# Performance work log

Measured on AMD Instinct MI355X. Metric: run time of the kernel, lower is better.

## Reference

```python
import jax, jax.numpy as jnp
import numpy as np

B, T, C = 64, 1024, 32   # batch, seq_len, n_embd
H, D = 4, 8              # num_heads, head_size (H*D == C)


def setup_inputs() -> dict:
    key = jax.random.key(0)
    ks = jax.random.split(key, 6)
    s = 0.02  # init scale for weights
    x = jax.random.normal(ks[0], (B, T, C), dtype=jnp.float32)
    Wq = jax.random.normal(ks[1], (H, C, D), dtype=jnp.float32) * s
    Wk = jax.random.normal(ks[2], (H, C, D), dtype=jnp.float32) * s
    Wv = jax.random.normal(ks[3], (H, C, D), dtype=jnp.float32) * s
    Wproj = jax.random.normal(ks[4], (H * D, C), dtype=jnp.float32) * s
    bproj = jnp.zeros((C,), dtype=jnp.float32)
    return {"x": x, "Wq": Wq, "Wk": Wk, "Wv": Wv, "Wproj": Wproj, "bproj": bproj}


def reference(x, Wq, Wk, Wv, Wproj, bproj):
    # All heads batched into one einsum instead of a Python loop over Head modules.
    q = jnp.einsum('btc,hcd->bhtd', x, Wq)
    k = jnp.einsum('btc,hcd->bhtd', x, Wk)
    v = jnp.einsum('btc,hcd->bhtd', x, Wv)
    scale = D ** -0.5
    att = jnp.einsum('bhtd,bhsd->bhts', q, k) * scale  # [B,H,T,T]
    causal = jnp.tril(jnp.ones((T, T), dtype=bool))
    att = jnp.where(causal, att, jnp.float32(-1e9))
    att = jax.nn.softmax(att, axis=-1)  # dropout omitted (eval mode)
    o = jnp.einsum('bhts,bhsd->bhtd', att, v)
    o = o.transpose(0, 2, 1, 3).reshape(B, T, H * D)  # concat heads on last dim
    return o @ Wproj + bproj  # final proj; output dropout omitted (eval mode)
```

## Files before the change

### kernel.cpp

```cpp
#include <hip/hip_runtime.h>
#include <math.h>

static constexpr int Bb = 64, Tt = 1024, Cc = 32, Hh = 4, Dd = 8;
static constexpr float QSCALE = 0.51006973f;

typedef _Float16 h2  __attribute__((ext_vector_type(2)));
typedef _Float16 v4h __attribute__((ext_vector_type(4)));
typedef float  f32x4 __attribute__((ext_vector_type(4)));

__device__ __forceinline__ h2 pkrtz(float a, float b) {
  return __builtin_bit_cast(h2, __builtin_amdgcn_cvt_pkrtz(a, b));
}

__device__ __forceinline__ float fdot2(h2 a, h2 b, float c) {
#if __has_builtin(__builtin_amdgcn_fdot2)
  return __builtin_amdgcn_fdot2(a, b, c, false);
#else
  return fmaf((float)a.x, (float)b.x, fmaf((float)a.y, (float)b.y, c));
#endif
}

__device__ __forceinline__ float frcp(float x) {
#if __has_builtin(__builtin_amdgcn_rcpf)
  return __builtin_amdgcn_rcpf(x);
#else
  return 1.0f / x;
#endif
}

__device__ __forceinline__ float bperm_f32(int src_lane, float v) {
  return __builtin_bit_cast(float,
      __builtin_amdgcn_ds_bpermute(src_lane << 2, __builtin_bit_cast(int, v)));
}

__device__ __forceinline__ h2 exp2h2(h2 s) {
  const h2 A3 = {(_Float16)0.05550411f, (_Float16)0.05550411f};
  const h2 A2 = {(_Float16)0.24022651f, (_Float16)0.24022651f};
  const h2 A1 = {(_Float16)0.69314718f, (_Float16)0.69314718f};
  const h2 ONE = {(_Float16)1.0f, (_Float16)1.0f};
  h2 t = A3 * s + A2;
  t = t * s + A1;
  t = t * s + ONE;
  return t;
}

union U4 { uint4 u; h2 h[4]; };
union P2 { uint2 u; h2 h[2]; v4h v; };

__global__ __launch_bounds__(256) void qkv_kernel(
    const float* __restrict__ x, const float* __restrict__ Wq,
    const float* __restrict__ Wk, const float* __restrict__ Wv,
    ushort* __restrict__ qo, ushort* __restrict__ ko, ushort* __restrict__ vo)
{
  __shared__ h2 wT[3][Hh][Dd][16];
  const int tid = threadIdx.x;
  {
    const int sh = tid >> 6, sd = (tid >> 3) & 7, c2b = tid & 7;
    const float* Ws[3] = {Wq, Wk, Wv};
#pragma unroll
    for (int mat = 0; mat < 3; ++mat) {
      const float* W = Ws[mat];
#pragma unroll
      for (int i = 0; i < 2; ++i) {
        const int c2 = c2b + 8 * i;
        const float w0 = W[(sh * Cc + 2 * c2) * Dd + sd];
        const float w1 = W[(sh * Cc + 2 * c2 + 1) * Dd + sd];
        wT[mat][sh][sd][c2] = pkrtz(w0, w1);
      }
    }
  }
  __syncthreads();

  const int h = tid >> 6, lane = tid & 63;
  const int b = blockIdx.x >> 3;
  const int t0 = ((blockIdx.x & 7) << 7) + lane;
  const int t1 = t0 + 64;
  const int bh = b * Hh + h;

  h2 xa[16], xb[16];
  {
    const float4* g0 = (const float4*)(x + ((long)b * Tt + t0) * Cc);
    const float4* g1 = (const float4*)(x + ((long)b * Tt + t1) * Cc);
#pragma unroll
    for (int i = 0; i < 8; ++i) {
      float4 va = g0[i], vb = g1[i];
      xa[2 * i]     = pkrtz(va.x, va.y);
      xa[2 * i + 1] = pkrtz(va.z, va.w);
      xb[2 * i]     = pkrtz(vb.x, vb.y);
      xb[2 * i + 1] = pkrtz(vb.z, vb.w);
    }
  }

#pragma unroll
  for (int mat = 0; mat < 3; ++mat) {
    float a0[Dd], a1[Dd];
#pragma unroll
    for (int d = 0; d < Dd; ++d) {
      float s0 = 0.f, s1 = 0.f;
#pragma unroll
      for (int c2 = 0; c2 < 16; ++c2) {
        const h2 w = wT[mat][h][d][c2];
        s0 = fdot2(xa[c2], w, s0);
        s1 = fdot2(xb[c2], w, s1);
      }
      a0[d] = s0; a1[d] = s1;
    }
    if (mat == 2) {
#pragma unroll
      for (int d = 0; d < Dd; ++d) {
        ((_Float16*)vo)[((long)bh * Dd + d) * Tt + t0] = (_Float16)a0[d];
        ((_Float16*)vo)[((long)bh * Dd + d) * Tt + t1] = (_Float16)a1[d];
      }
    } else {
      const float sc = (mat == 0) ? QSCALE : 1.0f;
      ushort* dst = (mat == 0) ? qo : ko;
      U4 u0, u1;
#pragma unroll
      for (int i = 0; i < 4; ++i) {
        u0.h[i] = pkrtz(a0[2 * i] * sc, a0[2 * i + 1] * sc);
        u1.h[i] = pkrtz(a1[2 * i] * sc, a1[2 * i + 1] * sc);
      }
      ((uint4*)(dst + ((long)bh * Tt + t0) * Dd))[0] = u0.u;
      ((uint4*)(dst + ((long)bh * Tt + t1) * Dd))[0] = u1.u;
    }
  }
}

__global__ __launch_bounds__(256, 4) void flash_kernel(
    const ushort* __restrict__ qg, const ushort* __restrict__ kg,
    const ushort* __restrict__ vg, ushort* __restrict__ og)
{
  __shared__ __align__(16) ushort ks[Tt * Dd];
  __shared__ __align__(16) ushort vs[9 * 1032];
  const int tid = threadIdx.x;
  const int bh = blockIdx.x & 255;
  const int g  = blockIdx.x >> 8;

  {
    const uint4* ksrc = (const uint4*)(kg + (long)bh * Tt * Dd);
    const uint4* vsrc = (const uint4*)(vg + (long)bh * Dd * Tt);
#pragma unroll
    for (int i = 0; i < 4; ++i)
      ((uint4*)ks)[tid + 256 * i] = ksrc[tid + 256 * i];
#pragma unroll
    for (int i = 0; i < 4; ++i) {
      const int idx = tid + 256 * i;
      const int d = idx >> 7, c8 = idx & 127;
      *(uint4*)(vs + d * 1032 + c8 * 8) = vsrc[idx];
    }
    if (tid < 128) {
      const unsigned one2 = 0x3C003C00u;
      *(uint4*)(vs + 8 * 1032 + tid * 8) = make_uint4(one2, one2, one2, one2);
    }
  }
  __syncthreads();

  const int lane = tid & 63;
  const int u  = __builtin_amdgcn_readfirstlane(tid >> 6);
  const int up = g * 4 + u;
  int rb[4];
  rb[0] = up; rb[1] = 31 - up; rb[2] = 32 + up; rb[3] = 63 - up;

  const int n = lane & 15, quad = lane >> 4;
  const ushort* kbase = ks + n * Dd + (quad & 1) * 4;
  const int vr = (n <= 8) ? n : (n - 8);
  const ushort* vbase = vs + vr * 1032 + quad * 4;

  h2 km0 = {(_Float16)((4 * quad + 0) <= n ? 1.f : 0.f),
            (_Float16)((4 * quad + 1) <= n ? 1.f : 0.f)};
  h2 km1 = {(_Float16)((4 * quad + 2) <= n ? 1.f : 0.f),
            (_Float16)((4 * quad + 3) <= n ? 1.f : 0.f)};

  P2 bq[4];
#pragma unroll
  for (int i = 0; i < 4; ++i) {
    uint2 r = *(const uint2*)(qg + ((long)bh * Tt + rb[i] * 16 + n) * Dd + (quad & 1) * 4);
    if (quad & 2) { r.x = 0; r.y = 0; }
    bq[i].u = r;
  }

  const f32x4 zero4 = {0.f, 0.f, 0.f, 0.f};
  f32x4 o[4];
#pragma unroll
  for (int i = 0; i < 4; ++i) o[i] = zero4;

  const int ctmax = 63 - up;
#pragma unroll 1
  for (int ct = 0; ct <= ctmax; ++ct) {
    P2 ak; ak.u = *(const uint2*)(kbase + ct * 128);
    const v4h bv = *(const v4h*)(vbase + ct * 16);
#pragma unroll
    for (int i = 0; i < 4; ++i) {
      if (ct <= rb[i]) {
        f32x4 s = __builtin_amdgcn_mfma_f32_16x16x16f16(ak.v, bq[i].v, zero4, 0, 0, 0);
        h2 p0 = exp2h2(pkrtz(s[0], s[1]));
        h2 p1 = exp2h2(pkrtz(s[2], s[3]));
        if (ct == rb[i]) { p0 *= km0; p1 *= km1; }
        P2 pf; pf.h[0] = p0; pf.h[1] = p1;
        o[i] = __builtin_amdgcn_mfma_f32_16x16x16f16(pf.v, bv, o[i], 0, 0, 0);
      }
    }
  }

  const int b = bh >> 2, h = bh & 3;
  const int lsrc = (lane & 48) | 8;
#pragma unroll
  for (int i = 0; i < 4; ++i) {
#pragma unroll
    for (int r = 0; r < 4; ++r) {
      const float l = bperm_f32(lsrc, o[i][r]);
      const float ov = o[i][r] * frcp(l);
      if (n < 8) {
        const int q = rb[i] * 16 + 4 * quad + r;
        ((_Float16*)og)[(((long)b * Tt + q) * Hh + h) * Dd + n] = (_Float16)ov;
      }
    }
  }
}

__global__ __launch_bounds__(256) void proj_kernel(
    const ushort* __restrict__ o_ws, const float* __restrict__ Wp,
    const float* __restrict__ bp, float* __restrict__ out)
{
  __shared__ h2 wT[Cc][16];
  __shared__ float bps[Cc];
  const int tid = threadIdx.x;
  {
    const int c = tid & 31, hp = tid >> 5;
#pragma unroll
    for (int i = 0; i < 2; ++i) {
      const int hd2 = hp + 8 * i;
      wT[c][hd2] = pkrtz(Wp[(2 * hd2) * Cc + c], Wp[(2 * hd2 + 1) * Cc + c]);
    }
    if (tid < Cc) bps[tid] = bp[tid];
  }
  __syncthreads();

  const int bt = blockIdx.x * 256 + tid;
  h2 orow[16];
  {
    const uint4* op = (const uint4*)(o_ws + (long)bt * Cc);
#pragma unroll
    for (int w = 0; w < 4; ++w) {
      U4 uu; uu.u = op[w];
#pragma unroll
      for (int i = 0; i < 4; ++i) orow[w * 4 + i] = uu.h[i];
    }
  }
  float acc[Cc];
#pragma unroll
  for (int c = 0; c < Cc; ++c) {
    float a = bps[c];
#pragma unroll
    for (int hd2 = 0; hd2 < 16; ++hd2) a = fdot2(orow[hd2], wT[c][hd2], a);
    acc[c] = a;
  }
  float4* og2 = (float4*)(out + (long)bt * Cc);
#pragma unroll
  for (int c4 = 0; c4 < 8; ++c4)
    og2[c4] = make_float4(acc[c4 * 4], acc[c4 * 4 + 1], acc[c4 * 4 + 2], acc[c4 * 4 + 3]);
}

extern "C" void kernel_launch(void* const* d_in, const int* in_sizes, int n_in,
                              void* d_out, int out_size, void* d_ws, size_t ws_size,
                              hipStream_t stream) {
  const float* x  = (const float*)d_in[0];
  const float* Wq = (const float*)d_in[1];
  const float* Wk = (const float*)d_in[2];
  const float* Wv = (const float*)d_in[3];
  const float* Wp = (const float*)d_in[4];
  const float* bp = (const float*)d_in[5];
  float* out = (float*)d_out;

  ushort* ws = (ushort*)d_ws;
  const long N = (long)Bb * Hh * Tt * Dd;
  ushort* q_ws = ws;
  ushort* k_ws = ws + N;
  ushort* v_ws = ws + 2 * N;
  ushort* o_ws = ws + 3 * N;

  qkv_kernel<<<Bb * Tt / 128, 256, 0, stream>>>(x, Wq, Wk, Wv, q_ws, k_ws, v_ws);
  flash_kernel<<<Bb * Hh * 4, 256, 0, stream>>>(q_ws, k_ws, v_ws, o_ws);
  proj_kernel<<<Bb * Tt / 256, 256, 0, stream>>>(o_ws, Wp, bp, out);
}
```

Baseline: 113.1 us.

## Fuse QKV projection into flash attention kernel, keeping Q/K/V in LDS

Merges the QKV projection kernel into the attention kernel. Each 512-thread block computes Q, K and V for its (batch, head) straight into shared memory, so the global round-trip of Q/K/V through workspace and one kernel launch go away. In exchange, every block recomputes the projection for its whole head (two blocks per head, so it is done twice) and reads x in full. LDS use also grows with the added Q buffer, which may lower occupancy.

```diff
diff --git a/kernel.cpp b/kernel.cpp
--- a/kernel.cpp
+++ b/kernel.cpp
@@ -47,36 +47,34 @@
 union U4 { uint4 u; h2 h[4]; };
 union P2 { uint2 u; h2 h[2]; v4h v; };
 
-__global__ __launch_bounds__(256) void qkv_kernel(
+__global__ __launch_bounds__(512, 4) void fused_attn_kernel(
     const float* __restrict__ x, const float* __restrict__ Wq,
     const float* __restrict__ Wk, const float* __restrict__ Wv,
-    ushort* __restrict__ qo, ushort* __restrict__ ko, ushort* __restrict__ vo)
+    ushort* __restrict__ og)
 {
-  __shared__ h2 wT[3][Hh][Dd][16];
+  __shared__ h2 wT[3][Dd][16];
+  __shared__ __align__(16) ushort ks[Tt * Dd];
+  __shared__ __align__(16) ushort vs[9 * 1032];
+  __shared__ __align__(16) ushort qs[Tt * Dd];
+
   const int tid = threadIdx.x;
-  {
-    const int sh = tid >> 6, sd = (tid >> 3) & 7, c2b = tid & 7;
-    const float* Ws[3] = {Wq, Wk, Wv};
-#pragma unroll
-    for (int mat = 0; mat < 3; ++mat) {
-      const float* W = Ws[mat];
-#pragma unroll
-      for (int i = 0; i < 2; ++i) {
-        const int c2 = c2b + 8 * i;
-        const float w0 = W[(sh * Cc + 2 * c2) * Dd + sd];
-        const float w1 = W[(sh * Cc + 2 * c2 + 1) * Dd + sd];
-        wT[mat][sh][sd][c2] = pkrtz(w0, w1);
-      }
-    }
-  }
-  __syncthreads();
-
-  const int h = tid >> 6, lane = tid & 63;
-  const int b = blockIdx.x >> 3;
-  const int t0 = ((blockIdx.x & 7) << 7) + lane;
-  const int t1 = t0 + 64;
-  const int bh = b * Hh + h;
-
+  const int bh = blockIdx.x & 255;
+  const int g  = blockIdx.x >> 8;
+  const int b = bh >> 2, h = bh & 3;
+
+  if (tid < 384) {
+    const int mat = tid >> 7, d = (tid >> 4) & 7, c2 = tid & 15;
+    const float* W = (mat == 0) ? Wq : (mat == 1) ? Wk : Wv;
+    const float w0 = W[(h * Cc + 2 * c2) * Dd + d];
+    const float w1 = W[(h * Cc + 2 * c2 + 1) * Dd + d];
+    wT[mat][d][c2] = pkrtz(w0, w1);
+  } else {
+    const int i = tid - 384;
+    const unsigned one2 = 0x3C003C00u;
+    *(uint4*)(vs + 8 * 1032 + i * 8) = make_uint4(one2, one2, one2, one2);
+  }
+
+  const int t0 = tid, t1 = tid + 512;
   h2 xa[16], xb[16];
   {
     const float4* g0 = (const float4*)(x + ((long)b * Tt + t0) * Cc);
@@ -90,6 +88,7 @@
       xb[2 * i + 1] = pkrtz(vb.z, vb.w);
     }
   }
+  __syncthreads();
 
 #pragma unroll
   for (int mat = 0; mat < 3; ++mat) {
@@ -99,7 +98,7 @@
       float s0 = 0.f, s1 = 0.f;
 #pragma unroll
       for (int c2 = 0; c2 < 16; ++c2) {
-        const h2 w = wT[mat][h][d][c2];
+        const h2 w = wT[mat][d][c2];
         s0 = fdot2(xa[c2], w, s0);
         s1 = fdot2(xb[c2], w, s1);
       }
@@ -108,58 +107,29 @@
     if (mat == 2) {
 #pragma unroll
       for (int d = 0; d < Dd; ++d) {
-        ((_Float16*)vo)[((long)bh * Dd + d) * Tt + t0] = (_Float16)a0[d];
-        ((_Float16*)vo)[((long)bh * Dd + d) * Tt + t1] = (_Float16)a1[d];
+        ((_Float16*)vs)[d * 1032 + t0] = (_Float16)a0[d];
+        ((_Float16*)vs)[d * 1032 + t1] = (_Float16)a1[d];
       }
     } else {
       const float sc = (mat == 0) ? QSCALE : 1.0f;
-      ushort* dst = (mat == 0) ? qo : ko;
+      ushort* dst = (mat == 0) ? qs : ks;
       U4 u0, u1;
 #pragma unroll
       for (int i = 0; i < 4; ++i) {
         u0.h[i] = pkrtz(a0[2 * i] * sc, a0[2 * i + 1] * sc);
         u1.h[i] = pkrtz(a1[2 * i] * sc, a1[2 * i + 1] * sc);
       }
-      ((uint4*)(dst + ((long)bh * Tt + t0) * Dd))[0] = u0.u;
-      ((uint4*)(dst + ((long)bh * Tt + t1) * Dd))[0] = u1.u;
-    }
-  }
-}
-
-__global__ __launch_bounds__(256, 4) void flash_kernel(
-    const ushort* __restrict__ qg, const ushort* __restrict__ kg,
-    const ushort* __restrict__ vg, ushort* __restrict__ og)
-{
-  __shared__ __align__(16) ushort ks[Tt * Dd];
-  __shared__ __align__(16) ushort vs[9 * 1032];
-  const int tid = threadIdx.x;
-  const int bh = blockIdx.x & 255;
-  const int g  = blockIdx.x >> 8;
-
-  {
-    const uint4* ksrc = (const uint4*)(kg + (long)bh * Tt * Dd);
-    const uint4* vsrc = (const uint4*)(vg + (long)bh * Dd * Tt);
-#pragma unroll
-    for (int i = 0; i < 4; ++i)
-      ((uint4*)ks)[tid + 256 * i] = ksrc[tid + 256 * i];
-#pragma unroll
-    for (int i = 0; i < 4; ++i) {
-      const int idx = tid + 256 * i;
-      const int d = idx >> 7, c8 = idx & 127;
-      *(uint4*)(vs + d * 1032 + c8 * 8) = vsrc[idx];
-    }
-    if (tid < 128) {
-      const unsigned one2 = 0x3C003C00u;
-      *(uint4*)(vs + 8 * 1032 + tid * 8) = make_uint4(one2, one2, one2, one2);
+      ((uint4*)(dst + t0 * Dd))[0] = u0.u;
+      ((uint4*)(dst + t1 * Dd))[0] = u1.u;
     }
   }
   __syncthreads();
 
   const int lane = tid & 63;
   const int u  = __builtin_amdgcn_readfirstlane(tid >> 6);
-  const int up = g * 4 + u;
+  const int w  = g * 8 + u;
   int rb[4];
-  rb[0] = up; rb[1] = 31 - up; rb[2] = 32 + up; rb[3] = 63 - up;
+  rb[0] = w; rb[1] = 31 - w; rb[2] = 32 + w; rb[3] = 63 - w;
 
   const int n = lane & 15, quad = lane >> 4;
   const ushort* kbase = ks + n * Dd + (quad & 1) * 4;
@@ -174,7 +144,7 @@
   P2 bq[4];
 #pragma unroll
   for (int i = 0; i < 4; ++i) {
-    uint2 r = *(const uint2*)(qg + ((long)bh * Tt + rb[i] * 16 + n) * Dd + (quad & 1) * 4);
+    uint2 r = *(const uint2*)(qs + (rb[i] * 16 + n) * Dd + (quad & 1) * 4);
     if (quad & 2) { r.x = 0; r.y = 0; }
     bq[i].u = r;
   }
@@ -184,7 +154,7 @@
 #pragma unroll
   for (int i = 0; i < 4; ++i) o[i] = zero4;
 
-  const int ctmax = 63 - up;
+  const int ctmax = 63 - w;
 #pragma unroll 1
   for (int ct = 0; ct <= ctmax; ++ct) {
     P2 ak; ak.u = *(const uint2*)(kbase + ct * 128);
@@ -202,7 +172,6 @@
     }
   }
 
-  const int b = bh >> 2, h = bh & 3;
   const int lsrc = (lane & 48) | 8;
 #pragma unroll
   for (int i = 0; i < 4; ++i) {
@@ -272,14 +241,8 @@
   const float* bp = (const float*)d_in[5];
   float* out = (float*)d_out;
 
-  ushort* ws = (ushort*)d_ws;
-  const long N = (long)Bb * Hh * Tt * Dd;
-  ushort* q_ws = ws;
-  ushort* k_ws = ws + N;
-  ushort* v_ws = ws + 2 * N;
-  ushort* o_ws = ws + 3 * N;
-
-  qkv_kernel<<<Bb * Tt / 128, 256, 0, stream>>>(x, Wq, Wk, Wv, q_ws, k_ws, v_ws);
-  flash_kernel<<<Bb * Hh * 4, 256, 0, stream>>>(q_ws, k_ws, v_ws, o_ws);
+  ushort* o_ws = (ushort*)d_ws;
+
+  fused_attn_kernel<<<Bb * Hh * 2, 512, 0, stream>>>(x, Wq, Wk, Wv, o_ws);
   proj_kernel<<<Bb * Tt / 256, 256, 0, stream>>>(o_ws, Wp, bp, out);
 }
```

New measurement: 113.8 us. Within noise of the previous version (+0.6%).
